# Performance work log

Hardware: AMD Instinct MI355X
Metric: run time of the kernel (lower is better)

Reference implementation:

```python
import jax, jax.numpy as jnp
import numpy as np

Q, N_EMBED, DIM = 4, 1024, 256
B, S = 8, 2048


def setup_inputs() -> dict:
    key = jax.random.key(0)
    k1, k2 = jax.random.split(key)
    x = jax.random.normal(k1, (B, S, DIM), dtype=jnp.float32)
    codebooks = jax.random.normal(k2, (Q, N_EMBED, DIM), dtype=jnp.float32)
    return {"x": x, "codebooks": codebooks}


def _vq_lookup(flat, embed):
    # flat: [M, D], embed: [K, D]
    dist = (jnp.sum(flat * flat, axis=-1, keepdims=True)
            - 2.0 * flat @ embed.T
            + jnp.sum(embed * embed, axis=-1))
    idx = jnp.argmin(dist, axis=-1)          # [M]
    quantize = embed[idx]                    # gather: [M, D]
    return quantize, idx


def reference(x, codebooks):
    sg = jax.lax.stop_gradient
    b, s, d = x.shape
    num_q = codebooks.shape[0]
    residual = x
    quantized_output = jnp.zeros_like(x)
    all_indices, all_losses = [], []
    for i in range(num_q):  # small fixed loop over quantizers
        flat = residual.reshape(-1, d)
        q, idx = _vq_lookup(flat, codebooks[i])
        q = q.reshape(b, s, d)
        # commitment loss: mse(sg(quantize), input)
        loss = jnp.mean((sg(q) - residual) ** 2)
        # straight-through estimator
        q_st = residual + sg(q - residual)
        residual = residual - q_st
        quantized_output = quantized_output + q_st
        all_indices.append(idx.reshape(b, s))
        all_losses.append(loss)
    return quantized_output, jnp.stack(all_indices), jnp.stack(all_losses)
```

## Files before the change

### kernel.cpp

```cpp
#include <hip/hip_runtime.h>

#define QQ   4
#define NE   1024
#define DIMD 256
#define MM   16384
#define TM   64
#define NW   8
#define CAP  32

typedef short v8s __attribute__((ext_vector_type(8)));
typedef float v4f __attribute__((ext_vector_type(4)));


struct SLds {
  double lossW[NW];
  float  residF[TM][DIMD + 4];
  unsigned short sX[TM][DIMD + 8];
  float  sBK[NE];
  float  av_s[TM];
  float  candD[TM][NW];
  float  thrS[TM];
  int    cnt[TM];
  int    candL[TM][CAP];
  float  dcD[TM][CAP];
  int    bcode[TM];
  float  fwD[NW];
  int    fwI[NW];
};

__device__ __forceinline__ unsigned short f2bf(float f) {
  unsigned u = __float_as_uint(f);
  return (unsigned short)((u + 0x7FFFu + ((u >> 16) & 1u)) >> 16);
}

__device__ __forceinline__ float np_sumsq_256_x32(const float* __restrict__ p,
                                                  int j) {
  const int bi = j >> 4, L = j & 15;
  const float* q = p + bi * 128 + L;
  float s0 = __fmul_rn(q[0], q[0]);
  float s1 = __fmul_rn(q[16], q[16]);
  float s2 = __fmul_rn(q[32], q[32]);
  float s3 = __fmul_rn(q[48], q[48]);
  float s4 = __fmul_rn(q[64], q[64]);
  float s5 = __fmul_rn(q[80], q[80]);
  float s6 = __fmul_rn(q[96], q[96]);
  float s7 = __fmul_rn(q[112], q[112]);
  float w = __fadd_rn(__fadd_rn(__fadd_rn(s0, s1), __fadd_rn(s2, s3)),
                      __fadd_rn(__fadd_rn(s4, s5), __fadd_rn(s6, s7)));
  float u  = __fadd_rn(w,  __shfl_down(w, 8, 64));
  float t  = __fadd_rn(u,  __shfl_down(u, 4, 64));
  float r2 = __fadd_rn(t,  __shfl_down(t, 2, 64));
  float bb = __fadd_rn(r2, __shfl_down(r2, 1, 64));
  return __fadd_rn(bb, __shfl_down(bb, 16, 64));
}

__device__ __forceinline__ float np_sumsq_256_x8(const float* __restrict__ p,
                                                 int j) {
  float blk[2];
  #pragma unroll
  for (int bi = 0; bi < 2; ++bi) {
    const float* base = p + bi * 128;
    float wpair[2];
    #pragma unroll
    for (int h = 0; h < 2; ++h) {
      const float* q = base + j + h * 8;
      float s0 = __fmul_rn(q[0], q[0]);
      float s1 = __fmul_rn(q[16], q[16]);
      float s2 = __fmul_rn(q[32], q[32]);
      float s3 = __fmul_rn(q[48], q[48]);
      float s4 = __fmul_rn(q[64], q[64]);
      float s5 = __fmul_rn(q[80], q[80]);
      float s6 = __fmul_rn(q[96], q[96]);
      float s7 = __fmul_rn(q[112], q[112]);
      wpair[h] = __fadd_rn(__fadd_rn(__fadd_rn(s0, s1), __fadd_rn(s2, s3)),
                           __fadd_rn(__fadd_rn(s4, s5), __fadd_rn(s6, s7)));
    }
    float u  = __fadd_rn(wpair[0], wpair[1]);
    float t  = __fadd_rn(u,  __shfl_down(u, 4, 64));
    float r2 = __fadd_rn(t,  __shfl_down(t, 2, 64));
    blk[bi]  = __fadd_rn(r2, __shfl_down(r2, 1, 64));
  }
  return __fadd_rn(blk[0], blk[1]);
}

__device__ __forceinline__ float np_dist_f4(const float* __restrict__ xp,
                                            const float* __restrict__ ep,
                                            float a, float b) {
  float m = 0.f;
  #pragma unroll 16
  for (int d4 = 0; d4 < DIMD / 4; ++d4) {
    const float4 xv = *(const float4*)(xp + d4 * 4);
    const float4 ev = *(const float4*)(ep + d4 * 4);
    m = fmaf(xv.x, ev.x, m);
    m = fmaf(xv.y, ev.y, m);
    m = fmaf(xv.z, ev.z, m);
    m = fmaf(xv.w, ev.w, m);
  }
  return __fadd_rn(__fsub_rn(a, __fmul_rn(2.0f, m)), b);
}

__global__ __launch_bounds__(256) void k_prep(const float* __restrict__ cb,
                                              unsigned short* __restrict__ cb16,
                                              float* __restrict__ bK,
                                              double* __restrict__ lossP,
                                              unsigned* __restrict__ done) {
  const int g = blockIdx.x * 256 + threadIdx.x;
  {
    const int i = g * 4;
    float4 f = *(const float4*)(cb + i);
    unsigned short t[4] = {f2bf(f.x), f2bf(f.y), f2bf(f.z), f2bf(f.w)};
    *(short4*)(cb16 + i) = *(short4*)t;
  }
  if (g < QQ * NE * 32) {
    const int row = g >> 5, j = g & 31;
    float b = np_sumsq_256_x32(cb + (size_t)row * DIMD, j);
    if (j == 0) bK[row] = b;
  }
  if (g < QQ * 64) lossP[g] = 0.0;
  if (g == 0) *done = 0u;
}

__global__ __launch_bounds__(512, 2) void k_fused(
    const float* __restrict__ x,
    const unsigned short* __restrict__ cb16a,
    const float* __restrict__ cba,
    const float* __restrict__ bKa,
    double* __restrict__ lossP,
    unsigned* __restrict__ doneCnt,
    float* __restrict__ out_q,
    float* __restrict__ idx_out,
    float* __restrict__ out_loss) {
  extern __shared__ char smem_raw[];
  SLds& S = *reinterpret_cast<SLds*>(smem_raw);

  const int tid  = threadIdx.x;
  const int lane = tid & 63;
  const int wv   = tid >> 6;
  const int rowBase = blockIdx.x * TM;
  const int r8  = tid >> 3;
  const int j8  = tid & 7;
  const int c0  = j8 * 32;
  const int m16  = lane & 15;
  const int quad = lane >> 4;

  {
    const float* xp = x + (size_t)(rowBase + r8) * DIMD + c0;
    #pragma unroll
    for (int h = 0; h < 8; ++h)
      *(float4*)&S.residF[r8][c0 + h * 4] = *(const float4*)(xp + h * 4);
  }
  __syncthreads();

  #pragma unroll 1
  for (int qi = 0; qi < QQ; ++qi) {
    const unsigned short* cb16 = cb16a + (size_t)qi * NE * DIMD;
    const float* cb = cba + (size_t)qi * NE * DIMD;
    const float* bK = bKa + (size_t)qi * NE;

    {
      float av = np_sumsq_256_x8(&S.residF[r8][0], j8);
      if (j8 == 0) S.av_s[r8] = av;
    }
    if (tid < TM) S.cnt[tid] = 0;
    S.sBK[tid] = bK[tid];
    S.sBK[tid + 512] = bK[tid + 512];
    {
      #pragma unroll
      for (int h = 0; h < 4; ++h) {
        const float* rp = &S.residF[r8][c0 + h * 8];
        const float4 f0 = *(const float4*)rp;
        const float4 f1 = *(const float4*)(rp + 4);
        unsigned short t[8] = {f2bf(f0.x), f2bf(f0.y), f2bf(f0.z), f2bf(f0.w),
                               f2bf(f1.x), f2bf(f1.y), f2bf(f1.z), f2bf(f1.w)};
        *(v8s*)&S.sX[r8][c0 + h * 8] = *(v8s*)t;
      }
    }
    __syncthreads();

    float bmx;
    {
      float bm = S.sBK[lane];
      #pragma unroll
      for (int t = 1; t < 16; ++t) bm = fmaxf(bm, S.sBK[lane + t * 64]);
      #pragma unroll
      for (int off = 32; off; off >>= 1) bm = fmaxf(bm, __shfl_xor(bm, off, 64));
      bmx = bm;
    }

    v4f acc[4][8];
    #pragma unroll
    for (int mt = 0; mt < 4; ++mt)
      #pragma unroll
      for (int ct = 0; ct < 8; ++ct) acc[mt][ct] = (v4f)(0.f);
    const unsigned short* bptr =
        cb16 + ((size_t)(wv * 128 + m16)) * DIMD + quad * 8;
    #pragma unroll
    for (int kc = 0; kc < 8; ++kc) {
      v8s bfr[8];
      #pragma unroll
      for (int ct = 0; ct < 8; ++ct)
        bfr[ct] = *(const v8s*)(bptr + (size_t)ct * 16 * DIMD + kc * 32);
      v8s afr[4];
      #pragma unroll
      for (int mt = 0; mt < 4; ++mt)
        afr[mt] = *(const v8s*)&S.sX[mt * 16 + m16][kc * 32 + quad * 8];
      #pragma unroll
      for (int ct = 0; ct < 8; ++ct) {
        #pragma unroll
        for (int mt = 0; mt < 4; ++mt)
          acc[mt][ct] = __builtin_amdgcn_mfma_f32_16x16x32_bf16(
              afr[mt], bfr[ct], acc[mt][ct], 0, 0, 0);
      }
    }

    float av16[4][4];
    #pragma unroll
    for (int mt = 0; mt < 4; ++mt)
      #pragma unroll
      for (int v = 0; v < 4; ++v) av16[mt][v] = S.av_s[mt * 16 + quad * 4 + v];
    #pragma unroll
    for (int ct = 0; ct < 8; ++ct) {
      const float bv = S.sBK[wv * 128 + ct * 16 + m16];
      #pragma unroll
      for (int mt = 0; mt < 4; ++mt)
        #pragma unroll
        for (int v = 0; v < 4; ++v)
          acc[mt][ct][v] = av16[mt][v] - 2.0f * acc[mt][ct][v] + bv;
    }

    #pragma unroll
    for (int mt = 0; mt < 4; ++mt) {
      float vmin[4];
      #pragma unroll
      for (int v = 0; v < 4; ++v) {
        vmin[v] = acc[mt][0][v];
        #pragma unroll
        for (int ct = 1; ct < 8; ++ct) vmin[v] = fminf(vmin[v], acc[mt][ct][v]);
        #pragma unroll
        for (int off = 1; off < 16; off <<= 1)
          vmin[v] = fminf(vmin[v], __shfl_xor(vmin[v], off, 64));
      }
      if (m16 == 0) {
        #pragma unroll
        for (int v = 0; v < 4; ++v)
          S.candD[mt * 16 + quad * 4 + v][wv] = vmin[v];
      }
    }
    __syncthreads();
    if (tid < TM) {
      float bd = S.candD[tid][0];
      #pragma unroll
      for (int w = 1; w < NW; ++w) bd = fminf(bd, S.candD[tid][w]);
      S.thrS[tid] = bd + 0.03125f * sqrtf(S.av_s[tid] * bmx) + 0.1f;
    }
    __syncthreads();

    #pragma unroll
    for (int ct = 0; ct < 8; ++ct) {
      const int code = wv * 128 + ct * 16 + m16;
      #pragma unroll
      for (int mt = 0; mt < 4; ++mt) {
        #pragma unroll
        for (int v = 0; v < 4; ++v) {
          const int row = mt * 16 + quad * 4 + v;
          if (acc[mt][ct][v] <= S.thrS[row]) {
            int pos = atomicAdd(&S.cnt[row], 1);
            if (pos < CAP) S.candL[row][pos] = code;
          }
        }
      }
    }
    __syncthreads();

    {
      const int n = (S.cnt[r8] <= CAP) ? S.cnt[r8] : 0;
      #pragma unroll
      for (int s = 0; s < 4; ++s) {
        const int ci = j8 + s * 8;
        if (ci < n) {
          const int code = S.candL[r8][ci];
          S.dcD[r8][ci] = np_dist_f4(&S.residF[r8][0],
                                     cb + (size_t)code * DIMD,
                                     S.av_s[r8], S.sBK[code]);
        }
      }
    }
    __syncthreads();

    for (int r = 0; r < TM; ++r) {
      if (S.cnt[r] > CAP) {
        const float* xp = &S.residF[r][0];
        const float a = S.av_s[r];
        float d1 = np_dist_f4(xp, cb + (size_t)tid * DIMD, a, S.sBK[tid]);
        float d2 = np_dist_f4(xp, cb + (size_t)(tid + 512) * DIMD, a, S.sBK[tid + 512]);
        int i1 = tid;
        if (d2 < d1) { d1 = d2; i1 = tid + 512; }
        #pragma unroll
        for (int off = 32; off; off >>= 1) {
          float vd = __shfl_xor(d1, off, 64);
          int vi = __shfl_xor(i1, off, 64);
          if (vd < d1 || (vd == d1 && vi < i1)) { d1 = vd; i1 = vi; }
        }
        if (lane == 0) { S.fwD[wv] = d1; S.fwI[wv] = i1; }
        __syncthreads();
        if (tid == 0) {
          float bd = S.fwD[0];
          int bi = S.fwI[0];
          #pragma unroll
          for (int w = 1; w < NW; ++w) {
            if (S.fwD[w] < bd || (S.fwD[w] == bd && S.fwI[w] < bi)) {
              bd = S.fwD[w]; bi = S.fwI[w];
            }
          }
          S.bcode[r] = bi;
        }
        __syncthreads();
      }
    }

    if (tid < TM) {
      if (S.cnt[tid] <= CAP) {
        float bd = 3.4e38f;
        int bi = 0x7fffffff;
        for (int ci = 0; ci < S.cnt[tid]; ++ci) {
          float d = S.dcD[tid][ci];
          int code = S.candL[tid][ci];
          if (d < bd || (d == bd && code < bi)) { bd = d; bi = code; }
        }
        S.bcode[tid] = bi;
      }
      idx_out[(size_t)qi * MM + rowBase + tid] = (float)S.bcode[tid];
    }
    __syncthreads();

    const int codeB = S.bcode[r8];
    double lsum = 0.0;
    #pragma unroll
    for (int h = 0; h < 8; ++h) {
      const int d = c0 + h * 4;
      const float4 ev = *(const float4*)(cb + (size_t)codeB * DIMD + d);
      const float4 rv = *(const float4*)&S.residF[r8][d];
      float t0 = __fsub_rn(ev.x, rv.x), u0 = __fadd_rn(rv.x, t0);
      float t1 = __fsub_rn(ev.y, rv.y), u1 = __fadd_rn(rv.y, t1);
      float t2 = __fsub_rn(ev.z, rv.z), u2 = __fadd_rn(rv.z, t2);
      float t3 = __fsub_rn(ev.w, rv.w), u3 = __fadd_rn(rv.w, t3);
      *(float4*)&S.residF[r8][d] =
          make_float4(__fsub_rn(rv.x, u0), __fsub_rn(rv.y, u1),
                      __fsub_rn(rv.z, u2), __fsub_rn(rv.w, u3));
      lsum += (double)__fmul_rn(t0, t0) + (double)__fmul_rn(t1, t1) +
              (double)__fmul_rn(t2, t2) + (double)__fmul_rn(t3, t3);
    }
    #pragma unroll
    for (int off = 32; off; off >>= 1) lsum += __shfl_xor(lsum, off, 64);
    if (lane == 0) S.lossW[wv] = lsum;
    __syncthreads();
    if (tid == 0) {
      double s = 0.0;
      #pragma unroll
      for (int w = 0; w < NW; ++w) s += S.lossW[w];
      atomicAdd(lossP + (size_t)qi * 64 + (blockIdx.x & 63), s);
    }
  }

  {
    const float* xp = x + (size_t)(rowBase + r8) * DIMD + c0;
    float* op = out_q + (size_t)(rowBase + r8) * DIMD + c0;
    #pragma unroll
    for (int h = 0; h < 8; ++h) {
      const float4 a = *(const float4*)(xp + h * 4);
      const float4 b = *(const float4*)&S.residF[r8][c0 + h * 4];
      *(float4*)(op + h * 4) =
          make_float4(__fsub_rn(a.x, b.x), __fsub_rn(a.y, b.y),
                      __fsub_rn(a.z, b.z), __fsub_rn(a.w, b.w));
    }
  }

  __syncthreads();
  if (tid == 0) {
    __threadfence();
    unsigned old = atomicAdd(doneCnt, 1u);
    S.cnt[0] = (old == (unsigned)(gridDim.x - 1)) ? 1 : 0;
  }
  __syncthreads();
  if (S.cnt[0] && tid < 64) {
    const int qi2 = tid >> 4;
    double s = 0.0;
    #pragma unroll
    for (int i = 0; i < 4; ++i)
      s += atomicAdd(lossP + (size_t)qi2 * 64 + (tid & 15) * 4 + i, 0.0);
    #pragma unroll
    for (int off = 8; off; off >>= 1) s += __shfl_down(s, off, 16);
    if ((tid & 15) == 0)
      out_loss[qi2] = (float)(s * (1.0 / (double)((size_t)MM * DIMD)));
  }
}

extern "C" void kernel_launch(void* const* d_in, const int* in_sizes, int n_in,
                              void* d_out, int out_size, void* d_ws, size_t ws_size,
                              hipStream_t stream) {
  const float* x = (const float*)d_in[0];
  const float* cb = (const float*)d_in[1];
  float* ws = (float*)d_ws;
  unsigned short* cb16 = (unsigned short*)ws;
  float* bK = ws + 524288;
  double* lossP = (double*)(ws + 528384);
  unsigned* done = (unsigned*)(ws + 528896);

  float* out = (float*)d_out;
  float* out_idx = out + (size_t)MM * DIMD;
  float* out_loss = out_idx + (size_t)QQ * MM;

  static bool attr_set = false;
  if (!attr_set) {
    hipFuncSetAttribute(reinterpret_cast<const void*>(k_fused),
                        hipFuncAttributeMaxDynamicSharedMemorySize,
                        (int)sizeof(SLds));
    attr_set = true;
  }

  k_prep<<<dim3(1024), dim3(256), 0, stream>>>(cb, cb16, bK, lossP, done);
  k_fused<<<dim3(MM / TM), dim3(512), sizeof(SLds), stream>>>(
      x, cb16, cb, bK, lossP, done, out, out_idx, out_loss);
}
```

Before: 331.7 us.

## Halve row tile to 32, fuse next-stage prep into residual update

Shrinks the per-block row tile from 64 to 32, doubling the grid and halving the MFMA accumulators per wave, and raises the candidate cap to 64. Each row is now handled by 16 threads. The sum-of-squares, bf16 conversion and bias load for the next quantizer are computed from registers inside the residual update, removing one barrier and a shared-memory re-read per stage. The trade-off is that each block streams the full codebook for half as many rows, so codebook traffic per row doubles.

After: 368.8 us. 11.2% more time.

```diff
diff --git a/kernel.cpp b/kernel.cpp
--- a/kernel.cpp
+++ b/kernel.cpp
@@ -4,9 +4,9 @@
 #define NE   1024
 #define DIMD 256
 #define MM   16384
-#define TM   64
+#define TM   32
 #define NW   8
-#define CAP  32
+#define CAP  64
 
 typedef short v8s __attribute__((ext_vector_type(8)));
 typedef float v4f __attribute__((ext_vector_type(4)));
@@ -54,33 +54,28 @@
   return __fadd_rn(bb, __shfl_down(bb, 16, 64));
 }
 
-__device__ __forceinline__ float np_sumsq_256_x8(const float* __restrict__ p,
-                                                 int j) {
-  float blk[2];
+__device__ __forceinline__ float np_sumsq_256_reg(const float* __restrict__ v) {
+  float s[16];
   #pragma unroll
-  for (int bi = 0; bi < 2; ++bi) {
-    const float* base = p + bi * 128;
-    float wpair[2];
-    #pragma unroll
-    for (int h = 0; h < 2; ++h) {
-      const float* q = base + j + h * 8;
-      float s0 = __fmul_rn(q[0], q[0]);
-      float s1 = __fmul_rn(q[16], q[16]);
-      float s2 = __fmul_rn(q[32], q[32]);
-      float s3 = __fmul_rn(q[48], q[48]);
-      float s4 = __fmul_rn(q[64], q[64]);
-      float s5 = __fmul_rn(q[80], q[80]);
-      float s6 = __fmul_rn(q[96], q[96]);
-      float s7 = __fmul_rn(q[112], q[112]);
-      wpair[h] = __fadd_rn(__fadd_rn(__fadd_rn(s0, s1), __fadd_rn(s2, s3)),
-                           __fadd_rn(__fadd_rn(s4, s5), __fadd_rn(s6, s7)));
-    }
-    float u  = __fadd_rn(wpair[0], wpair[1]);
-    float t  = __fadd_rn(u,  __shfl_down(u, 4, 64));
-    float r2 = __fadd_rn(t,  __shfl_down(t, 2, 64));
-    blk[bi]  = __fadd_rn(r2, __shfl_down(r2, 1, 64));
-  }
-  return __fadd_rn(blk[0], blk[1]);
+  for (int L = 0; L < 16; ++L) s[L] = __fmul_rn(v[L], v[L]);
+  #pragma unroll
+  for (int m = 1; m <= 4; m <<= 1) {
+    #pragma unroll
+    for (int L = 0; L < 16; ++L) {
+      float o = __shfl_xor(s[L], m, 64);
+      s[L] = __fadd_rn(s[L], o);
+    }
+  }
+  float u[8], t[4], r2[2];
+  #pragma unroll
+  for (int L = 0; L < 8; ++L) u[L] = __fadd_rn(s[L], s[L + 8]);
+  #pragma unroll
+  for (int L = 0; L < 4; ++L) t[L] = __fadd_rn(u[L], u[L + 4]);
+  #pragma unroll
+  for (int L = 0; L < 2; ++L) r2[L] = __fadd_rn(t[L], t[L + 2]);
+  float blk = __fadd_rn(r2[0], r2[1]);
+  float o = __shfl_xor(blk, 8, 64);
+  return __fadd_rn(blk, o);
 }
 
 __device__ __forceinline__ float np_dist_f4(const float* __restrict__ xp,
@@ -137,45 +132,41 @@
   const int lane = tid & 63;
   const int wv   = tid >> 6;
   const int rowBase = blockIdx.x * TM;
-  const int r8  = tid >> 3;
-  const int j8  = tid & 7;
-  const int c0  = j8 * 32;
+  const int r16 = tid >> 4;
+  const int j16 = tid & 15;
+  const int d0  = j16 * 16;
   const int m16  = lane & 15;
   const int quad = lane >> 4;
 
   {
-    const float* xp = x + (size_t)(rowBase + r8) * DIMD + c0;
-    #pragma unroll
-    for (int h = 0; h < 8; ++h)
-      *(float4*)&S.residF[r8][c0 + h * 4] = *(const float4*)(xp + h * 4);
-  }
+    const float* xp = x + (size_t)(rowBase + r16) * DIMD + d0;
+    float rn[16];
+    #pragma unroll
+    for (int h = 0; h < 4; ++h) {
+      const float4 a = *(const float4*)(xp + h * 4);
+      rn[h * 4 + 0] = a.x; rn[h * 4 + 1] = a.y;
+      rn[h * 4 + 2] = a.z; rn[h * 4 + 3] = a.w;
+      *(float4*)&S.residF[r16][d0 + h * 4] = a;
+    }
+    #pragma unroll
+    for (int h = 0; h < 2; ++h) {
+      unsigned short t8[8];
+      #pragma unroll
+      for (int k = 0; k < 8; ++k) t8[k] = f2bf(rn[h * 8 + k]);
+      *(v8s*)&S.sX[r16][d0 + h * 8] = *(v8s*)t8;
+    }
+    float av = np_sumsq_256_reg(rn);
+    if (j16 == 0) S.av_s[r16] = av;
+  }
+  if (tid < TM) S.cnt[tid] = 0;
+  S.sBK[tid] = bKa[tid];
+  S.sBK[tid + 512] = bKa[tid + 512];
   __syncthreads();
 
   #pragma unroll 1
   for (int qi = 0; qi < QQ; ++qi) {
     const unsigned short* cb16 = cb16a + (size_t)qi * NE * DIMD;
     const float* cb = cba + (size_t)qi * NE * DIMD;
-    const float* bK = bKa + (size_t)qi * NE;
-
-    {
-      float av = np_sumsq_256_x8(&S.residF[r8][0], j8);
-      if (j8 == 0) S.av_s[r8] = av;
-    }
-    if (tid < TM) S.cnt[tid] = 0;
-    S.sBK[tid] = bK[tid];
-    S.sBK[tid + 512] = bK[tid + 512];
-    {
-      #pragma unroll
-      for (int h = 0; h < 4; ++h) {
-        const float* rp = &S.residF[r8][c0 + h * 8];
-        const float4 f0 = *(const float4*)rp;
-        const float4 f1 = *(const float4*)(rp + 4);
-        unsigned short t[8] = {f2bf(f0.x), f2bf(f0.y), f2bf(f0.z), f2bf(f0.w),
-                               f2bf(f1.x), f2bf(f1.y), f2bf(f1.z), f2bf(f1.w)};
-        *(v8s*)&S.sX[r8][c0 + h * 8] = *(v8s*)t;
-      }
-    }
-    __syncthreads();
 
     float bmx;
     {
@@ -187,9 +178,9 @@
       bmx = bm;
     }
 
-    v4f acc[4][8];
-    #pragma unroll
-    for (int mt = 0; mt < 4; ++mt)
+    v4f acc[2][8];
+    #pragma unroll
+    for (int mt = 0; mt < 2; ++mt)
       #pragma unroll
       for (int ct = 0; ct < 8; ++ct) acc[mt][ct] = (v4f)(0.f);
     const unsigned short* bptr =
@@ -200,36 +191,32 @@
       #pragma unroll
       for (int ct = 0; ct < 8; ++ct)
         bfr[ct] = *(const v8s*)(bptr + (size_t)ct * 16 * DIMD + kc * 32);
-      v8s afr[4];
-      #pragma unroll
-      for (int mt = 0; mt < 4; ++mt)
-        afr[mt] = *(const v8s*)&S.sX[mt * 16 + m16][kc * 32 + quad * 8];
+      v8s a0 = *(const v8s*)&S.sX[m16][kc * 32 + quad * 8];
+      v8s a1 = *(const v8s*)&S.sX[16 + m16][kc * 32 + quad * 8];
       #pragma unroll
       for (int ct = 0; ct < 8; ++ct) {
-        #pragma unroll
-        for (int mt = 0; mt < 4; ++mt)
-          acc[mt][ct] = __builtin_amdgcn_mfma_f32_16x16x32_bf16(
-              afr[mt], bfr[ct], acc[mt][ct], 0, 0, 0);
-      }
-    }
-
-    float av16[4][4];
-    #pragma unroll
-    for (int mt = 0; mt < 4; ++mt)
-      #pragma unroll
-      for (int v = 0; v < 4; ++v) av16[mt][v] = S.av_s[mt * 16 + quad * 4 + v];
+        acc[0][ct] = __builtin_amdgcn_mfma_f32_16x16x32_bf16(a0, bfr[ct], acc[0][ct], 0, 0, 0);
+        acc[1][ct] = __builtin_amdgcn_mfma_f32_16x16x32_bf16(a1, bfr[ct], acc[1][ct], 0, 0, 0);
+      }
+    }
+
+    float av8[2][4];
+    #pragma unroll
+    for (int mt = 0; mt < 2; ++mt)
+      #pragma unroll
+      for (int v = 0; v < 4; ++v) av8[mt][v] = S.av_s[mt * 16 + quad * 4 + v];
     #pragma unroll
     for (int ct = 0; ct < 8; ++ct) {
       const float bv = S.sBK[wv * 128 + ct * 16 + m16];
       #pragma unroll
-      for (int mt = 0; mt < 4; ++mt)
+      for (int mt = 0; mt < 2; ++mt)
         #pragma unroll
         for (int v = 0; v < 4; ++v)
-          acc[mt][ct][v] = av16[mt][v] - 2.0f * acc[mt][ct][v] + bv;
-    }
-
-    #pragma unroll
-    for (int mt = 0; mt < 4; ++mt) {
+          acc[mt][ct][v] = av8[mt][v] - 2.0f * acc[mt][ct][v] + bv;
+    }
+
+    #pragma unroll
+    for (int mt = 0; mt < 2; ++mt) {
       float vmin[4];
       #pragma unroll
       for (int v = 0; v < 4; ++v) {
@@ -242,8 +229,7 @@
       }
       if (m16 == 0) {
         #pragma unroll
-        for (int v = 0; v < 4; ++v)
-          S.candD[mt * 16 + quad * 4 + v][wv] = vmin[v];
+        for (int v = 0; v < 4; ++v) S.candD[mt * 16 + quad * 4 + v][wv] = vmin[v];
       }
     }
     __syncthreads();
@@ -259,7 +245,7 @@
     for (int ct = 0; ct < 8; ++ct) {
       const int code = wv * 128 + ct * 16 + m16;
       #pragma unroll
-      for (int mt = 0; mt < 4; ++mt) {
+      for (int mt = 0; mt < 2; ++mt) {
         #pragma unroll
         for (int v = 0; v < 4; ++v) {
           const int row = mt * 16 + quad * 4 + v;
@@ -273,15 +259,15 @@
     __syncthreads();
 
     {
-      const int n = (S.cnt[r8] <= CAP) ? S.cnt[r8] : 0;
-      #pragma unroll
-      for (int s = 0; s < 4; ++s) {
-        const int ci = j8 + s * 8;
+      const int n = (S.cnt[r16] <= CAP) ? S.cnt[r16] : 0;
+      #pragma unroll
+      for (int k = 0; k < 4; ++k) {
+        const int ci = j16 + k * 16;
         if (ci < n) {
-          const int code = S.candL[r8][ci];
-          S.dcD[r8][ci] = np_dist_f4(&S.residF[r8][0],
-                                     cb + (size_t)code * DIMD,
-                                     S.av_s[r8], S.sBK[code]);
+          const int code = S.candL[r16][ci];
+          S.dcD[r16][ci] = np_dist_f4(&S.residF[r16][0],
+                                      cb + (size_t)code * DIMD,
+                                      S.av_s[r16], S.sBK[code]);
         }
       }
     }
@@ -333,26 +319,45 @@
     }
     __syncthreads();
 
-    const int codeB = S.bcode[r8];
-    double lsum = 0.0;
-    #pragma unroll
-    for (int h = 0; h < 8; ++h) {
-      const int d = c0 + h * 4;
-      const float4 ev = *(const float4*)(cb + (size_t)codeB * DIMD + d);
-      const float4 rv = *(const float4*)&S.residF[r8][d];
-      float t0 = __fsub_rn(ev.x, rv.x), u0 = __fadd_rn(rv.x, t0);
-      float t1 = __fsub_rn(ev.y, rv.y), u1 = __fadd_rn(rv.y, t1);
-      float t2 = __fsub_rn(ev.z, rv.z), u2 = __fadd_rn(rv.z, t2);
-      float t3 = __fsub_rn(ev.w, rv.w), u3 = __fadd_rn(rv.w, t3);
-      *(float4*)&S.residF[r8][d] =
-          make_float4(__fsub_rn(rv.x, u0), __fsub_rn(rv.y, u1),
-                      __fsub_rn(rv.z, u2), __fsub_rn(rv.w, u3));
-      lsum += (double)__fmul_rn(t0, t0) + (double)__fmul_rn(t1, t1) +
-              (double)__fmul_rn(t2, t2) + (double)__fmul_rn(t3, t3);
-    }
-    #pragma unroll
-    for (int off = 32; off; off >>= 1) lsum += __shfl_xor(lsum, off, 64);
-    if (lane == 0) S.lossW[wv] = lsum;
+    {
+      const int codeB = S.bcode[r16];
+      double lsum = 0.0;
+      float rn[16];
+      #pragma unroll
+      for (int h = 0; h < 4; ++h) {
+        const int d = d0 + h * 4;
+        const float4 ev = *(const float4*)(cb + (size_t)codeB * DIMD + d);
+        const float4 rv = *(const float4*)&S.residF[r16][d];
+        float t0 = __fsub_rn(ev.x, rv.x), u0 = __fadd_rn(rv.x, t0);
+        float t1 = __fsub_rn(ev.y, rv.y), u1 = __fadd_rn(rv.y, t1);
+        float t2 = __fsub_rn(ev.z, rv.z), u2 = __fadd_rn(rv.z, t2);
+        float t3 = __fsub_rn(ev.w, rv.w), u3 = __fadd_rn(rv.w, t3);
+        const float4 nv = make_float4(__fsub_rn(rv.x, u0), __fsub_rn(rv.y, u1),
+                                      __fsub_rn(rv.z, u2), __fsub_rn(rv.w, u3));
+        *(float4*)&S.residF[r16][d] = nv;
+        rn[h * 4 + 0] = nv.x; rn[h * 4 + 1] = nv.y;
+        rn[h * 4 + 2] = nv.z; rn[h * 4 + 3] = nv.w;
+        lsum += (double)__fmul_rn(t0, t0) + (double)__fmul_rn(t1, t1) +
+                (double)__fmul_rn(t2, t2) + (double)__fmul_rn(t3, t3);
+      }
+      if (qi < QQ - 1) {
+        #pragma unroll
+        for (int h = 0; h < 2; ++h) {
+          unsigned short t8[8];
+          #pragma unroll
+          for (int k = 0; k < 8; ++k) t8[k] = f2bf(rn[h * 8 + k]);
+          *(v8s*)&S.sX[r16][d0 + h * 8] = *(v8s*)t8;
+        }
+        float av = np_sumsq_256_reg(rn);
+        if (j16 == 0) S.av_s[r16] = av;
+        S.sBK[tid] = bKa[(size_t)(qi + 1) * NE + tid];
+        S.sBK[tid + 512] = bKa[(size_t)(qi + 1) * NE + tid + 512];
+      }
+      if (tid < TM) S.cnt[tid] = 0;
+      #pragma unroll
+      for (int off = 32; off; off >>= 1) lsum += __shfl_xor(lsum, off, 64);
+      if (lane == 0) S.lossW[wv] = lsum;
+    }
     __syncthreads();
     if (tid == 0) {
       double s = 0.0;
@@ -363,12 +368,12 @@
   }
 
   {
-    const float* xp = x + (size_t)(rowBase + r8) * DIMD + c0;
-    float* op = out_q + (size_t)(rowBase + r8) * DIMD + c0;
-    #pragma unroll
-    for (int h = 0; h < 8; ++h) {
+    const float* xp = x + (size_t)(rowBase + r16) * DIMD + d0;
+    float* op = out_q + (size_t)(rowBase + r16) * DIMD + d0;
+    #pragma unroll
+    for (int h = 0; h < 4; ++h) {
       const float4 a = *(const float4*)(xp + h * 4);
-      const float4 b = *(const float4*)&S.residF[r8][c0 + h * 4];
+      const float4 b = *(const float4*)&S.residF[r16][d0 + h * 4];
       *(float4*)(op + h * 4) =
           make_float4(__fsub_rn(a.x, b.x), __fsub_rn(a.y, b.y),
                       __fsub_rn(a.z, b.z), __fsub_rn(a.w, b.w));
```
